# Kernel optimization log

Measured on AMD Instinct MI355X. Metric: run time of the kernel, lower is better.

## Reference

```python
import jax, jax.numpy as jnp
import numpy as np

N_NODES = 200000
N_EDGES = 600000
D_IN = 128
D_HID = 128
D_OUT = 100
NUM_GRAPHS = 2048
BN_EPS = 1e-5


def setup_inputs() -> dict:
    key = jax.random.key(0)
    ks = jax.random.split(key, 10)
    atom_features = jax.random.normal(ks[0], (N_NODES, D_IN), dtype=jnp.float32)
    edge_index = jax.random.randint(ks[1], (2, N_EDGES), 0, N_NODES, dtype=jnp.int32)
    batch = jnp.sort(jax.random.randint(ks[2], (N_NODES,), 0, NUM_GRAPHS, dtype=jnp.int32))
    s1 = 1.0 / np.sqrt(D_IN)
    s2 = 1.0 / np.sqrt(D_HID)
    return {
        "atom_features": atom_features,
        "edge_index": edge_index,
        "batch": batch,
        "num_graphs": NUM_GRAPHS,
        "W1": jax.random.uniform(ks[3], (D_IN, D_HID), jnp.float32, -s1, s1),
        "b1": jnp.zeros((D_HID,), jnp.float32),
        "gamma": jnp.ones((D_HID,), jnp.float32),
        "beta": jnp.zeros((D_HID,), jnp.float32),
        "W2": jax.random.uniform(ks[4], (D_HID, D_OUT), jnp.float32, -s2, s2),
        "b2": jnp.zeros((D_OUT,), jnp.float32),
    }


def gcn_conv(x, src, dst, W, b, num_nodes):
    # GCNConv: D^{-1/2} (A + I) D^{-1/2} X W + b  (self-loops already appended to src/dst)
    h = x @ W  # [N, F]
    deg = jax.ops.segment_sum(jnp.ones_like(dst, dtype=h.dtype), dst, num_segments=num_nodes)
    dinv = jnp.where(deg > 0, jax.lax.rsqrt(deg), 0.0)
    norm = dinv[src] * dinv[dst]  # [E+N]
    msg = h[src] * norm[:, None]
    out = jax.ops.segment_sum(msg, dst, num_segments=num_nodes)
    return out + b


def batch_norm(x, gamma, beta):
    mu = jnp.mean(x, axis=0)
    var = jnp.mean(jnp.square(x - mu), axis=0)
    return (x - mu) * jax.lax.rsqrt(var + BN_EPS) * gamma + beta


def reference(atom_features, edge_index, batch, num_graphs, W1, b1, gamma, beta, W2, b2):
    n = atom_features.shape[0]
    loops = jnp.arange(n, dtype=edge_index.dtype)
    src = jnp.concatenate([edge_index[0], loops])
    dst = jnp.concatenate([edge_index[1], loops])
    x = gcn_conv(atom_features, src, dst, W1, b1, n)
    x = batch_norm(x, gamma, beta)
    x = jax.nn.relu(x)  # dropout is a no-op in eval
    x = gcn_conv(x, src, dst, W2, b2, n)
    # global max pool by graph id
    return jax.ops.segment_max(x, batch, num_segments=num_graphs)
```

## Files before the change

kernel.cpp:

```cpp
#include <hip/hip_runtime.h>
#include <hip/hip_bf16.h>

#define D_HID 128
#define D_OUT 100
#define BN_EPS 1e-5f
#define XP 136
#define ROWB 272

typedef short bf16x8 __attribute__((ext_vector_type(8)));
typedef float f32x4 __attribute__((ext_vector_type(4)));

__device__ __forceinline__ unsigned fmap(float f) {
    unsigned u = __float_as_uint(f);
    return (u & 0x80000000u) ? ~u : (u | 0x80000000u);
}
__device__ __forceinline__ float funmap(unsigned u) {
    return __uint_as_float((u & 0x80000000u) ? (u ^ 0x80000000u) : ~u);
}
#define NEG_INF_MAPPED 0x007FFFFFu

__device__ __forceinline__ unsigned short f2bf(float f) {
    unsigned u = __float_as_uint(f);
    return (unsigned short)((u + 0x7fffu + ((u >> 16) & 1u)) >> 16);
}
__device__ __forceinline__ unsigned packbf2(float x, float y) {
    return (unsigned)f2bf(x) | ((unsigned)f2bf(y) << 16);
}
__device__ __forceinline__ float2 unpackbf2(unsigned v) {
    float2 r;
    r.x = __uint_as_float(v << 16);
    r.y = __uint_as_float(v & 0xffff0000u);
    return r;
}

__global__ __launch_bounds__(256) void init_k(int* deg, int* cursor, unsigned* pool,
                                              float* bnsum, float* bnsq, int N, int P) {
    int i = blockIdx.x * 256 + threadIdx.x;
    if (i < N) { deg[i] = 0; cursor[i] = 0; }
    if (i < P) pool[i] = NEG_INF_MAPPED;
    if (i < 128) { bnsum[i] = 0.f; bnsq[i] = 0.f; }
}

__global__ __launch_bounds__(256) void deg_k(const int* __restrict__ dst, int* deg, int E) {
    int e = blockIdx.x * 256 + threadIdx.x;
    if (e < E) atomicAdd(&deg[dst[e]], 1);
}

#define SCAN_EPB 1024
__global__ __launch_bounds__(256) void scan1_k(const int* __restrict__ deg, int* __restrict__ off,
                                               int* __restrict__ btot, int N) {
    __shared__ int ts[256];
    int base = blockIdx.x * SCAN_EPB + threadIdx.x * 4;
    int v[4];
    int s = 0;
#pragma unroll
    for (int j = 0; j < 4; ++j) { int idx = base + j; v[j] = (idx < N) ? deg[idx] : 0; s += v[j]; }
    ts[threadIdx.x] = s;
    __syncthreads();
    for (int d = 1; d < 256; d <<= 1) {
        int t = (threadIdx.x >= d) ? ts[threadIdx.x - d] : 0;
        __syncthreads();
        ts[threadIdx.x] += t;
        __syncthreads();
    }
    int excl = ts[threadIdx.x] - s;
#pragma unroll
    for (int j = 0; j < 4; ++j) { int idx = base + j; if (idx < N) off[idx] = excl; excl += v[j]; }
    if (threadIdx.x == 255) btot[blockIdx.x] = ts[255];
}

__global__ __launch_bounds__(256) void scan2_k(int* btot, int nb, int* off, int N, int E) {
    __shared__ int ts[256];
    int v = (threadIdx.x < nb) ? btot[threadIdx.x] : 0;
    ts[threadIdx.x] = v;
    __syncthreads();
    for (int d = 1; d < 256; d <<= 1) {
        int t = (threadIdx.x >= d) ? ts[threadIdx.x - d] : 0;
        __syncthreads();
        ts[threadIdx.x] += t;
        __syncthreads();
    }
    if (threadIdx.x < nb) btot[threadIdx.x] = ts[threadIdx.x] - v;
    if (threadIdx.x == 0) off[N] = E;
}

__global__ __launch_bounds__(256) void scan3_dinv_k(int* off, const int* __restrict__ btot,
                                                    const int* __restrict__ deg,
                                                    float* __restrict__ dinv, int N) {
    int i = blockIdx.x * 256 + threadIdx.x;
    if (i < N) {
        off[i] += btot[i / SCAN_EPB];
        dinv[i] = rsqrtf((float)(1 + deg[i]));
    }
}

__global__ __launch_bounds__(256) void fill_k(const int* __restrict__ src, const int* __restrict__ dst,
                                              const int* __restrict__ off, int* cursor,
                                              int* __restrict__ csr, int E) {
    int e = blockIdx.x * 256 + threadIdx.x;
    if (e < E) {
        int d = dst[e];
        int p = atomicAdd(&cursor[d], 1);
        csr[off[d] + p] = src[e];
    }
}

__global__ __launch_bounds__(256) void prepW_k(const float* __restrict__ W1,
                                               const float* __restrict__ W2,
                                               unsigned short* __restrict__ W1t,
                                               unsigned short* __restrict__ W2t) {
    int t = blockIdx.x * 256 + threadIdx.x;
    if (t < 16384) { int n = t >> 7, k = t & 127; W1t[t] = f2bf(W1[k * 128 + n]); }
    if (t < 14336) { int c = t >> 7, k = t & 127; W2t[t] = (c < D_OUT) ? f2bf(W2[k * D_OUT + c]) : (unsigned short)0; }
}

__global__ __launch_bounds__(256) void gemm1_k(const float* __restrict__ X,
                                               const unsigned short* __restrict__ W1t,
                                               const float* __restrict__ dinv,
                                               unsigned* __restrict__ H, int N) {
    __shared__ char smem[64 * ROWB + 128 * ROWB];
    char* Xs = smem;
    char* Wt = smem + 64 * ROWB;
    int tid = threadIdx.x;
    int row0 = blockIdx.x * 64;
    {
        const uint4* Wg = (const uint4*)W1t;
#pragma unroll
        for (int i = 0; i < 8; ++i) {
            int idx = i * 256 + tid;
            uint4 u = Wg[idx];
            *(uint4*)(Wt + (idx >> 4) * ROWB + (idx & 15) * 16) = u;
        }
    }
    {
        const float4* Xg = (const float4*)X;
#pragma unroll
        for (int i = 0; i < 8; ++i) {
            int idx = i * 256 + tid;
            int r = idx >> 5, c4 = idx & 31;
            int grow = row0 + r; if (grow >= N) grow = N - 1;
            float4 v = Xg[(long long)grow * 32 + c4];
            uint2 o; o.x = packbf2(v.x, v.y); o.y = packbf2(v.z, v.w);
            *(uint2*)(Xs + r * ROWB + c4 * 8) = o;
        }
    }
    __syncthreads();
    int w = tid >> 6, l = tid & 63;
    int arow = w * 16 + (l & 15);
    int koff = (l >> 4) * 16;
    f32x4 acc[8];
#pragma unroll
    for (int ct = 0; ct < 8; ++ct)
#pragma unroll
        for (int r = 0; r < 4; ++r) acc[ct][r] = 0.f;
#pragma unroll
    for (int ks = 0; ks < 4; ++ks) {
        int kb = ks * 64 + koff;
        bf16x8 a = *(const bf16x8*)(Xs + arow * ROWB + kb);
#pragma unroll
        for (int ct = 0; ct < 8; ++ct) {
            bf16x8 b = *(const bf16x8*)(Wt + (ct * 16 + (l & 15)) * ROWB + kb);
            acc[ct] = __builtin_amdgcn_mfma_f32_16x16x32_bf16(a, b, acc[ct], 0, 0, 0);
        }
    }
    __syncthreads();
    {
        int crow0 = w * 16 + (l >> 4) * 4;
        int ccol = l & 15;
#pragma unroll
        for (int ct = 0; ct < 8; ++ct)
#pragma unroll
            for (int r = 0; r < 4; ++r)
                *(unsigned short*)(Xs + (crow0 + r) * ROWB + (ct * 16 + ccol) * 2) = f2bf(acc[ct][r]);
    }
    __syncthreads();
#pragma unroll
    for (int i = 0; i < 16; ++i) {
        int idx = i * 256 + tid;
        int r = idx >> 6, cu = idx & 63;
        int grow = row0 + r;
        if (grow < N) {
            float2 f = unpackbf2(*(unsigned*)(Xs + r * ROWB + cu * 4));
            float d = dinv[grow];
            H[(long long)grow * 64 + cu] = packbf2(f.x * d, f.y * d);
        }
    }
}

#define A1_FLUSH_ADV()                                                  \
    do {                                                                \
        float ox = dncur * acc.x, oy = dncur * acc.y;                   \
        X1[(long long)n * 64 + lane] = packbf2(ox, oy);                 \
        bs.x += ox; bs.y += oy;                                         \
        bq.x += ox * ox; bq.y += oy * oy;                               \
        ++n;                                                            \
        nend = off[n + 1];                                              \
        dncur = dinv[n];                                                \
        acc = unpackbf2(hnext);                                         \
        int np_ = (n + 1 < N) ? (n + 1) : (N - 1);                      \
        hnext = H[(long long)np_ * 64 + lane];                          \
    } while (0)

__global__ __launch_bounds__(256) void agg1_k(const unsigned* __restrict__ H,
                                              const int* __restrict__ off,
                                              const int* __restrict__ csr,
                                              const float* __restrict__ dinv,
                                              unsigned* __restrict__ X1,
                                              float* bnsum, float* bnsq,
                                              int N, int chunk) {
    int grp = blockIdx.x * 4 + (threadIdx.x >> 6);
    int lane = threadIdx.x & 63;
    int n0 = grp * chunk;
    int n1 = n0 + chunk; if (n1 > N) n1 = N;
    float2 bs; bs.x = 0.f; bs.y = 0.f;
    float2 bq; bq.x = 0.f; bq.y = 0.f;
    if (n0 < n1) {
        int n = n0;
        int i = off[n0];
        int eend = off[n1];
        int nend = off[n0 + 1];
        float dncur = dinv[n0];
        float2 acc = unpackbf2(H[(long long)n0 * 64 + lane]);
        int np0 = (n0 + 1 < N) ? (n0 + 1) : (N - 1);
        unsigned hnext = H[(long long)np0 * 64 + lane];
        while (i + 4 <= eend) {
            int s0 = csr[i], s1 = csr[i + 1], s2 = csr[i + 2], s3 = csr[i + 3];
            unsigned g0 = H[(long long)s0 * 64 + lane];
            unsigned g1 = H[(long long)s1 * 64 + lane];
            unsigned g2 = H[(long long)s2 * 64 + lane];
            unsigned g3 = H[(long long)s3 * 64 + lane];
            while (i >= nend) A1_FLUSH_ADV();
            { float2 f = unpackbf2(g0); acc.x += f.x; acc.y += f.y; }
            while (i + 1 >= nend) A1_FLUSH_ADV();
            { float2 f = unpackbf2(g1); acc.x += f.x; acc.y += f.y; }
            while (i + 2 >= nend) A1_FLUSH_ADV();
            { float2 f = unpackbf2(g2); acc.x += f.x; acc.y += f.y; }
            while (i + 3 >= nend) A1_FLUSH_ADV();
            { float2 f = unpackbf2(g3); acc.x += f.x; acc.y += f.y; }
            i += 4;
        }
        while (i < eend) {
            int s0 = csr[i];
            unsigned g0 = H[(long long)s0 * 64 + lane];
            while (i >= nend) A1_FLUSH_ADV();
            { float2 f = unpackbf2(g0); acc.x += f.x; acc.y += f.y; }
            ++i;
        }
        for (;;) {
            float ox = dncur * acc.x, oy = dncur * acc.y;
            X1[(long long)n * 64 + lane] = packbf2(ox, oy);
            bs.x += ox; bs.y += oy;
            bq.x += ox * ox; bq.y += oy * oy;
            ++n;
            if (n >= n1) break;
            dncur = dinv[n];
            acc = unpackbf2(hnext);
            int np_ = (n + 1 < N) ? (n + 1) : (N - 1);
            hnext = H[(long long)np_ * 64 + lane];
        }
    }
    __shared__ float2 ls[256], lq[256];
    ls[threadIdx.x] = bs; lq[threadIdx.x] = bq;
    __syncthreads();
    if (threadIdx.x < 64) {
        float2 s = ls[threadIdx.x], q = lq[threadIdx.x];
#pragma unroll
        for (int j = 64; j < 256; j += 64) {
            float2 a = ls[threadIdx.x + j], b = lq[threadIdx.x + j];
            s.x += a.x; s.y += a.y; q.x += b.x; q.y += b.y;
        }
        atomicAdd(&bnsum[threadIdx.x * 2 + 0], s.x);
        atomicAdd(&bnsum[threadIdx.x * 2 + 1], s.y);
        atomicAdd(&bnsq[threadIdx.x * 2 + 0], q.x);
        atomicAdd(&bnsq[threadIdx.x * 2 + 1], q.y);
    }
}

__global__ __launch_bounds__(128) void bnfinal_k(const float* bnsum, const float* bnsq,
                                                 const float* __restrict__ gamma,
                                                 const float* __restrict__ beta,
                                                 float* scale, float* shift, int N) {
    int c = threadIdx.x;
    float mu = bnsum[c] / (float)N;
    float var = bnsq[c] / (float)N - mu * mu;
    var = var > 0.f ? var : 0.f;
    float sc = gamma[c] * rsqrtf(var + BN_EPS);
    scale[c] = sc;
    shift[c] = beta[c] - mu * sc;
}

__global__ __launch_bounds__(256) void gemm2_k(const unsigned* __restrict__ X1,
                                               const unsigned short* __restrict__ W2t,
                                               const float* __restrict__ scale,
                                               const float* __restrict__ shift,
                                               const float* __restrict__ dinv,
                                               unsigned* __restrict__ H2, int N) {
    __shared__ char smem[64 * ROWB + 112 * ROWB];
    __shared__ float scs[128], shs[128];
    char* Xs = smem;
    char* Wt = smem + 64 * ROWB;
    int tid = threadIdx.x;
    int row0 = blockIdx.x * 64;
    if (tid < 128) { scs[tid] = scale[tid]; shs[tid] = shift[tid]; }
    {
        const uint4* Wg = (const uint4*)W2t;
#pragma unroll
        for (int i = 0; i < 7; ++i) {
            int idx = i * 256 + tid;
            uint4 u = Wg[idx];
            *(uint4*)(Wt + (idx >> 4) * ROWB + (idx & 15) * 16) = u;
        }
    }
    __syncthreads();
    {
        const uint4* Xg = (const uint4*)X1;
#pragma unroll
        for (int i = 0; i < 4; ++i) {
            int idx = i * 256 + tid;
            int r = idx >> 4, kc = idx & 15;
            int grow = row0 + r; if (grow >= N) grow = N - 1;
            uint4 u = Xg[(long long)grow * 16 + kc];
            uint4 o;
#pragma unroll
            for (int jj = 0; jj < 4; ++jj) {
                float2 f = unpackbf2((&u.x)[jj]);
                int k = kc * 8 + jj * 2;
                float v0 = f.x * scs[k] + shs[k];
                float v1 = f.y * scs[k + 1] + shs[k + 1];
                (&o.x)[jj] = packbf2(v0 > 0.f ? v0 : 0.f, v1 > 0.f ? v1 : 0.f);
            }
            *(uint4*)(Xs + r * ROWB + kc * 16) = o;
        }
    }
    __syncthreads();
    int w = tid >> 6, l = tid & 63;
    int arow = w * 16 + (l & 15);
    int koff = (l >> 4) * 16;
    f32x4 acc[7];
#pragma unroll
    for (int ct = 0; ct < 7; ++ct)
#pragma unroll
        for (int r = 0; r < 4; ++r) acc[ct][r] = 0.f;
#pragma unroll
    for (int ks = 0; ks < 4; ++ks) {
        int kb = ks * 64 + koff;
        bf16x8 a = *(const bf16x8*)(Xs + arow * ROWB + kb);
#pragma unroll
        for (int ct = 0; ct < 7; ++ct) {
            bf16x8 b = *(const bf16x8*)(Wt + (ct * 16 + (l & 15)) * ROWB + kb);
            acc[ct] = __builtin_amdgcn_mfma_f32_16x16x32_bf16(a, b, acc[ct], 0, 0, 0);
        }
    }
    __syncthreads();
    {
        int crow0 = w * 16 + (l >> 4) * 4;
        int ccol = l & 15;
#pragma unroll
        for (int ct = 0; ct < 7; ++ct)
#pragma unroll
            for (int r = 0; r < 4; ++r)
                *(unsigned short*)(Xs + (crow0 + r) * ROWB + (ct * 16 + ccol) * 2) = f2bf(acc[ct][r]);
    }
    __syncthreads();
#pragma unroll
    for (int i = 0; i < 13; ++i) {
        int idx = i * 256 + tid;
        if (idx < 3200) {
            int r = idx / 50, cu = idx - r * 50;
            int grow = row0 + r;
            if (grow < N) {
                float2 f = unpackbf2(*(unsigned*)(Xs + r * ROWB + cu * 4));
                float d = dinv[grow];
                H2[(long long)grow * 50 + cu] = packbf2(f.x * d, f.y * d);
            }
        }
    }
}

#define NINF (-__builtin_inff())
#define A2_FLUSH_ADV()                                                  \
    do {                                                                \
        float vx_ = dncur * acc.x + bf.x, vy_ = dncur * acc.y + bf.y;   \
        int gb_ = batch[n];                                             \
        if (gb_ != gcur) {                                              \
            long long pb_ = (long long)gcur * D_OUT + lane * 2;         \
            atomicMax(&pool[pb_], fmap(mx));                            \
            atomicMax(&pool[pb_ + 1], fmap(my));                        \
            gcur = gb_; mx = NINF; my = NINF;                           \
        }                                                               \
        mx = mx > vx_ ? mx : vx_; my = my > vy_ ? my : vy_;             \
        ++n;                                                            \
        nend = off[n + 1];                                              \
        dncur = dinv[n];                                                \
        acc = unpackbf2(hnext);                                         \
        int np_ = (n + 1 < N) ? (n + 1) : (N - 1);                      \
        hnext = H2[(long long)np_ * 50 + lane];                         \
    } while (0)

__global__ __launch_bounds__(256) void agg2pool_k(const unsigned* __restrict__ H2,
                                                  const int* __restrict__ off,
                                                  const int* __restrict__ csr,
                                                  const float* __restrict__ dinv,
                                                  const int* __restrict__ batch,
                                                  const float* __restrict__ b2,
                                                  unsigned* __restrict__ pool,
                                                  int N, int chunk) {
    int grp = blockIdx.x * 4 + (threadIdx.x >> 6);
    int lane = threadIdx.x & 63;
    if (lane >= 50) return;
    int n0 = grp * chunk;
    int n1 = n0 + chunk; if (n1 > N) n1 = N;
    if (n0 >= n1) return;
    float2 bf = ((const float2*)b2)[lane];
    float mx = NINF, my = NINF;
    int gcur = batch[n0];
    int n = n0;
    int i = off[n0];
    int eend = off[n1];
    int nend = off[n0 + 1];
    float dncur = dinv[n0];
    float2 acc = unpackbf2(H2[(long long)n0 * 50 + lane]);
    int np0 = (n0 + 1 < N) ? (n0 + 1) : (N - 1);
    unsigned hnext = H2[(long long)np0 * 50 + lane];
    while (i + 4 <= eend) {
        int s0 = csr[i], s1 = csr[i + 1], s2 = csr[i + 2], s3 = csr[i + 3];
        unsigned g0 = H2[(long long)s0 * 50 + lane];
        unsigned g1 = H2[(long long)s1 * 50 + lane];
        unsigned g2 = H2[(long long)s2 * 50 + lane];
        unsigned g3 = H2[(long long)s3 * 50 + lane];
        while (i >= nend) A2_FLUSH_ADV();
        { float2 f = unpackbf2(g0); acc.x += f.x; acc.y += f.y; }
        while (i + 1 >= nend) A2_FLUSH_ADV();
        { float2 f = unpackbf2(g1); acc.x += f.x; acc.y += f.y; }
        while (i + 2 >= nend) A2_FLUSH_ADV();
        { float2 f = unpackbf2(g2); acc.x += f.x; acc.y += f.y; }
        while (i + 3 >= nend) A2_FLUSH_ADV();
        { float2 f = unpackbf2(g3); acc.x += f.x; acc.y += f.y; }
        i += 4;
    }
    while (i < eend) {
        int s0 = csr[i];
        unsigned g0 = H2[(long long)s0 * 50 + lane];
        while (i >= nend) A2_FLUSH_ADV();
        { float2 f = unpackbf2(g0); acc.x += f.x; acc.y += f.y; }
        ++i;
    }
    for (;;) {
        float vx_ = dncur * acc.x + bf.x, vy_ = dncur * acc.y + bf.y;
        int gb_ = batch[n];
        if (gb_ != gcur) {
            long long pb_ = (long long)gcur * D_OUT + lane * 2;
            atomicMax(&pool[pb_], fmap(mx));
            atomicMax(&pool[pb_ + 1], fmap(my));
            gcur = gb_; mx = NINF; my = NINF;
        }
        mx = mx > vx_ ? mx : vx_; my = my > vy_ ? my : vy_;
        ++n;
        if (n >= n1) break;
        dncur = dinv[n];
        acc = unpackbf2(hnext);
        int np_ = (n + 1 < N) ? (n + 1) : (N - 1);
        hnext = H2[(long long)np_ * 50 + lane];
    }
    long long pb = (long long)gcur * D_OUT + lane * 2;
    atomicMax(&pool[pb], fmap(mx));
    atomicMax(&pool[pb + 1], fmap(my));
}

__global__ __launch_bounds__(256) void pool_final_k(const unsigned* __restrict__ pool,
                                                    float* __restrict__ out, int P) {
    int i = blockIdx.x * 256 + threadIdx.x;
    if (i < P) out[i] = funmap(pool[i]);
}

extern "C" void kernel_launch(void* const* d_in, const int* in_sizes, int n_in,
                              void* d_out, int out_size, void* d_ws, size_t ws_size,
                              hipStream_t stream) {
    const float* X     = (const float*)d_in[0];
    const int*   eidx  = (const int*)d_in[1];
    const int*   batch = (const int*)d_in[2];
    const float* W1    = (const float*)d_in[4];
    const float* gamma = (const float*)d_in[6];
    const float* beta  = (const float*)d_in[7];
    const float* W2    = (const float*)d_in[8];
    const float* b2    = (const float*)d_in[9];

    const int N = in_sizes[0] / D_HID;
    const int E = in_sizes[1] / 2;
    const int P = out_size;
    const int* src = eidx;
    const int* dst = eidx + E;

    char* p = (char*)d_ws;
    auto alloc = [&](size_t bytes) { char* q = p; p += (bytes + 255) & ~(size_t)255; return q; };
    int*      deg    = (int*)alloc((size_t)N * 4);
    int*      cursor = (int*)alloc((size_t)N * 4);
    int*      off    = (int*)alloc((size_t)(N + 1) * 4);
    int*      btot   = (int*)alloc(256 * 4);
    int*      csr    = (int*)alloc((size_t)E * 4);
    float*    dinv   = (float*)alloc((size_t)N * 4);
    float*    bnsum  = (float*)alloc(128 * 4);
    float*    bnsq   = (float*)alloc(128 * 4);
    float*    scale  = (float*)alloc(128 * 4);
    float*    shift  = (float*)alloc(128 * 4);
    unsigned short* W1t = (unsigned short*)alloc(16384 * 2);
    unsigned short* W2t = (unsigned short*)alloc(14336 * 2);
    unsigned* pool   = (unsigned*)alloc((size_t)P * 4);
    unsigned* A      = (unsigned*)alloc((size_t)N * 128 * 2);
    unsigned* B      = (unsigned*)alloc((size_t)N * 128 * 2);

    const int nb1 = (N + SCAN_EPB - 1) / SCAN_EPB;
    const int initN = (N > P ? N : P);

    init_k<<<(initN + 255) / 256, 256, 0, stream>>>(deg, cursor, pool, bnsum, bnsq, N, P);
    deg_k<<<(E + 255) / 256, 256, 0, stream>>>(dst, deg, E);
    scan1_k<<<nb1, 256, 0, stream>>>(deg, off, btot, N);
    scan2_k<<<1, 256, 0, stream>>>(btot, nb1, off, N, E);
    scan3_dinv_k<<<(N + 255) / 256, 256, 0, stream>>>(off, btot, deg, dinv, N);
    fill_k<<<(E + 255) / 256, 256, 0, stream>>>(src, dst, off, cursor, csr, E);
    prepW_k<<<64, 256, 0, stream>>>(W1, W2, W1t, W2t);

    const int nblk_g = (N + 63) / 64;
    gemm1_k<<<nblk_g, 256, 0, stream>>>(X, W1t, dinv, A, N);

    const int nblk_agg = 2048;
    const int ngrp = nblk_agg * 4;
    const int chunk = (N + ngrp - 1) / ngrp;
    agg1_k<<<nblk_agg, 256, 0, stream>>>(A, off, csr, dinv, B, bnsum, bnsq, N, chunk);
    bnfinal_k<<<1, 128, 0, stream>>>(bnsum, bnsq, gamma, beta, scale, shift, N);

    gemm2_k<<<nblk_g, 256, 0, stream>>>(B, W2t, scale, shift, dinv, A, N);

    agg2pool_k<<<nblk_agg, 256, 0, stream>>>(A, off, csr, dinv, batch, b2, pool, N, chunk);
    pool_final_k<<<(P + 255) / 256, 256, 0, stream>>>(pool, (float*)d_out, P);
}
```

Measured before the change: 313.1 us.

## Pad CSR to even degree and gather two edges per wavefront with half-wave lanes

Each node's CSR neighbour list is padded to an even length, using a dummy node whose feature row is zero. Each wavefront then processes edge pairs: each half-wave gathers one source row with 8-byte loads, and the two halves are summed with a cross-lane shuffle before the node's output is written. The goal is to halve the number of serial gather iterations and widen the memory accesses in both aggregation kernels. The cost is extra padding work, a new pad kernel, idle lanes in the second layer's 25-of-32 layout, and shuffles on every node flush.

Measured after the change: 419.4 us. 34.0% more time.

```diff
diff --git a/kernel.cpp b/kernel.cpp
--- a/kernel.cpp
+++ b/kernel.cpp
@@ -32,13 +32,20 @@
     r.y = __uint_as_float(v & 0xffff0000u);
     return r;
 }
+__device__ __forceinline__ f32x4 unpack4(uint2 u) {
+    float2 a = unpackbf2(u.x), b = unpackbf2(u.y);
+    f32x4 r; r[0] = a.x; r[1] = a.y; r[2] = b.x; r[3] = b.y;
+    return r;
+}
 
 __global__ __launch_bounds__(256) void init_k(int* deg, int* cursor, unsigned* pool,
-                                              float* bnsum, float* bnsq, int N, int P) {
+                                              float* bnsum, float* bnsq,
+                                              unsigned* Hpad, int N, int P) {
     int i = blockIdx.x * 256 + threadIdx.x;
     if (i < N) { deg[i] = 0; cursor[i] = 0; }
     if (i < P) pool[i] = NEG_INF_MAPPED;
     if (i < 128) { bnsum[i] = 0.f; bnsq[i] = 0.f; }
+    if (i < 64) Hpad[i] = 0;
 }
 
 __global__ __launch_bounds__(256) void deg_k(const int* __restrict__ dst, int* deg, int E) {
@@ -54,7 +61,12 @@
     int v[4];
     int s = 0;
 #pragma unroll
-    for (int j = 0; j < 4; ++j) { int idx = base + j; v[j] = (idx < N) ? deg[idx] : 0; s += v[j]; }
+    for (int j = 0; j < 4; ++j) {
+        int idx = base + j;
+        int d = (idx < N) ? deg[idx] : 0;
+        v[j] = d + (d & 1);
+        s += v[j];
+    }
     ts[threadIdx.x] = s;
     __syncthreads();
     for (int d = 1; d < 256; d <<= 1) {
@@ -69,7 +81,7 @@
     if (threadIdx.x == 255) btot[blockIdx.x] = ts[255];
 }
 
-__global__ __launch_bounds__(256) void scan2_k(int* btot, int nb, int* off, int N, int E) {
+__global__ __launch_bounds__(256) void scan2_k(int* btot, int nb, int* off, int N) {
     __shared__ int ts[256];
     int v = (threadIdx.x < nb) ? btot[threadIdx.x] : 0;
     ts[threadIdx.x] = v;
@@ -81,7 +93,7 @@
         __syncthreads();
     }
     if (threadIdx.x < nb) btot[threadIdx.x] = ts[threadIdx.x] - v;
-    if (threadIdx.x == 0) off[N] = E;
+    if (threadIdx.x == 255) off[N] = ts[255];
 }
 
 __global__ __launch_bounds__(256) void scan3_dinv_k(int* off, const int* __restrict__ btot,
@@ -102,6 +114,15 @@
         int d = dst[e];
         int p = atomicAdd(&cursor[d], 1);
         csr[off[d] + p] = src[e];
+    }
+}
+
+__global__ __launch_bounds__(256) void pad_k(const int* __restrict__ deg, const int* __restrict__ off,
+                                             int* __restrict__ csr, int N) {
+    int i = blockIdx.x * 256 + threadIdx.x;
+    if (i < N) {
+        int d = deg[i];
+        if (d & 1) csr[off[i] + d] = N;
     }
 }
 
@@ -187,100 +208,127 @@
     }
 }
 
-#define A1_FLUSH_ADV()                                                  \
-    do {                                                                \
-        float ox = dncur * acc.x, oy = dncur * acc.y;                   \
-        X1[(long long)n * 64 + lane] = packbf2(ox, oy);                 \
-        bs.x += ox; bs.y += oy;                                         \
-        bq.x += ox * ox; bq.y += oy * oy;                               \
-        ++n;                                                            \
-        nend = off[n + 1];                                              \
-        dncur = dinv[n];                                                \
-        acc = unpackbf2(hnext);                                         \
-        int np_ = (n + 1 < N) ? (n + 1) : (N - 1);                      \
-        hnext = H[(long long)np_ * 64 + lane];                          \
+#define A1_FLUSH_ADV()                                                      \
+    do {                                                                    \
+        f32x4 tot;                                                          \
+        tot[0] = acc[0] + __shfl(acc[0], lane + 32);                        \
+        tot[1] = acc[1] + __shfl(acc[1], lane + 32);                        \
+        tot[2] = acc[2] + __shfl(acc[2], lane + 32);                        \
+        tot[3] = acc[3] + __shfl(acc[3], lane + 32);                        \
+        if (lo) {                                                           \
+            f32x4 ox;                                                       \
+            ox[0] = dncur * tot[0]; ox[1] = dncur * tot[1];                 \
+            ox[2] = dncur * tot[2]; ox[3] = dncur * tot[3];                 \
+            uint2 o; o.x = packbf2(ox[0], ox[1]); o.y = packbf2(ox[2], ox[3]); \
+            X1v[(long long)n * 32 + hl] = o;                                \
+            bs += ox; bq += ox * ox;                                        \
+        }                                                                   \
+        ++n;                                                                \
+        pn = off[n + 1] >> 1;                                               \
+        dncur = dinv[n];                                                    \
+        if (lo) acc = unpack4(hnext); else { acc[0]=0.f;acc[1]=0.f;acc[2]=0.f;acc[3]=0.f; } \
+        int np_ = (n + 1 < N) ? (n + 1) : (N - 1);                          \
+        hnext = Hv[(long long)np_ * 32 + hl];                               \
     } while (0)
 
-__global__ __launch_bounds__(256) void agg1_k(const unsigned* __restrict__ H,
+__global__ __launch_bounds__(256) void agg1_k(const uint2* __restrict__ Hv,
                                               const int* __restrict__ off,
-                                              const int* __restrict__ csr,
+                                              const int2* __restrict__ csr2,
                                               const float* __restrict__ dinv,
-                                              unsigned* __restrict__ X1,
+                                              uint2* __restrict__ X1v,
                                               float* bnsum, float* bnsq,
                                               int N, int chunk) {
     int grp = blockIdx.x * 4 + (threadIdx.x >> 6);
     int lane = threadIdx.x & 63;
+    int hl = lane & 31;
+    bool lo = lane < 32;
     int n0 = grp * chunk;
     int n1 = n0 + chunk; if (n1 > N) n1 = N;
-    float2 bs; bs.x = 0.f; bs.y = 0.f;
-    float2 bq; bq.x = 0.f; bq.y = 0.f;
+    f32x4 bs; bs[0]=0.f;bs[1]=0.f;bs[2]=0.f;bs[3]=0.f;
+    f32x4 bq = bs;
     if (n0 < n1) {
         int n = n0;
-        int i = off[n0];
-        int eend = off[n1];
-        int nend = off[n0 + 1];
+        int pi = off[n0] >> 1;
+        int pe = off[n1] >> 1;
+        int pn = off[n0 + 1] >> 1;
         float dncur = dinv[n0];
-        float2 acc = unpackbf2(H[(long long)n0 * 64 + lane]);
+        f32x4 acc;
+        {
+            uint2 hs = Hv[(long long)n0 * 32 + hl];
+            if (lo) acc = unpack4(hs); else { acc[0]=0.f;acc[1]=0.f;acc[2]=0.f;acc[3]=0.f; }
+        }
         int np0 = (n0 + 1 < N) ? (n0 + 1) : (N - 1);
-        unsigned hnext = H[(long long)np0 * 64 + lane];
-        while (i + 4 <= eend) {
-            int s0 = csr[i], s1 = csr[i + 1], s2 = csr[i + 2], s3 = csr[i + 3];
-            unsigned g0 = H[(long long)s0 * 64 + lane];
-            unsigned g1 = H[(long long)s1 * 64 + lane];
-            unsigned g2 = H[(long long)s2 * 64 + lane];
-            unsigned g3 = H[(long long)s3 * 64 + lane];
-            while (i >= nend) A1_FLUSH_ADV();
-            { float2 f = unpackbf2(g0); acc.x += f.x; acc.y += f.y; }
-            while (i + 1 >= nend) A1_FLUSH_ADV();
-            { float2 f = unpackbf2(g1); acc.x += f.x; acc.y += f.y; }
-            while (i + 2 >= nend) A1_FLUSH_ADV();
-            { float2 f = unpackbf2(g2); acc.x += f.x; acc.y += f.y; }
-            while (i + 3 >= nend) A1_FLUSH_ADV();
-            { float2 f = unpackbf2(g3); acc.x += f.x; acc.y += f.y; }
-            i += 4;
-        }
-        while (i < eend) {
-            int s0 = csr[i];
-            unsigned g0 = H[(long long)s0 * 64 + lane];
-            while (i >= nend) A1_FLUSH_ADV();
-            { float2 f = unpackbf2(g0); acc.x += f.x; acc.y += f.y; }
-            ++i;
+        uint2 hnext = Hv[(long long)np0 * 32 + hl];
+        while (pi + 4 <= pe) {
+            int2 e0 = csr2[pi], e1 = csr2[pi + 1], e2 = csr2[pi + 2], e3 = csr2[pi + 3];
+            int s0 = lo ? e0.x : e0.y, s1 = lo ? e1.x : e1.y;
+            int s2 = lo ? e2.x : e2.y, s3 = lo ? e3.x : e3.y;
+            uint2 g0 = Hv[(long long)s0 * 32 + hl];
+            uint2 g1 = Hv[(long long)s1 * 32 + hl];
+            uint2 g2 = Hv[(long long)s2 * 32 + hl];
+            uint2 g3 = Hv[(long long)s3 * 32 + hl];
+            while (pi >= pn) A1_FLUSH_ADV();
+            acc += unpack4(g0);
+            while (pi + 1 >= pn) A1_FLUSH_ADV();
+            acc += unpack4(g1);
+            while (pi + 2 >= pn) A1_FLUSH_ADV();
+            acc += unpack4(g2);
+            while (pi + 3 >= pn) A1_FLUSH_ADV();
+            acc += unpack4(g3);
+            pi += 4;
+        }
+        while (pi < pe) {
+            int2 e0 = csr2[pi];
+            int s0 = lo ? e0.x : e0.y;
+            uint2 g0 = Hv[(long long)s0 * 32 + hl];
+            while (pi >= pn) A1_FLUSH_ADV();
+            acc += unpack4(g0);
+            ++pi;
         }
         for (;;) {
-            float ox = dncur * acc.x, oy = dncur * acc.y;
-            X1[(long long)n * 64 + lane] = packbf2(ox, oy);
-            bs.x += ox; bs.y += oy;
-            bq.x += ox * ox; bq.y += oy * oy;
+            f32x4 tot;
+            tot[0] = acc[0] + __shfl(acc[0], lane + 32);
+            tot[1] = acc[1] + __shfl(acc[1], lane + 32);
+            tot[2] = acc[2] + __shfl(acc[2], lane + 32);
+            tot[3] = acc[3] + __shfl(acc[3], lane + 32);
+            if (lo) {
+                f32x4 ox;
+                ox[0] = dncur * tot[0]; ox[1] = dncur * tot[1];
+                ox[2] = dncur * tot[2]; ox[3] = dncur * tot[3];
+                uint2 o; o.x = packbf2(ox[0], ox[1]); o.y = packbf2(ox[2], ox[3]);
+                X1v[(long long)n * 32 + hl] = o;
+                bs += ox; bq += ox * ox;
+            }
             ++n;
             if (n >= n1) break;
             dncur = dinv[n];
-            acc = unpackbf2(hnext);
+            if (lo) acc = unpack4(hnext); else { acc[0]=0.f;acc[1]=0.f;acc[2]=0.f;acc[3]=0.f; }
             int np_ = (n + 1 < N) ? (n + 1) : (N - 1);
-            hnext = H[(long long)np_ * 64 + lane];
-        }
-    }
-    __shared__ float2 ls[256], lq[256];
+            hnext = Hv[(long long)np_ * 32 + hl];
+        }
+    }
+    __shared__ f32x4 ls[256], lq[256];
     ls[threadIdx.x] = bs; lq[threadIdx.x] = bq;
     __syncthreads();
-    if (threadIdx.x < 64) {
-        float2 s = ls[threadIdx.x], q = lq[threadIdx.x];
-#pragma unroll
-        for (int j = 64; j < 256; j += 64) {
-            float2 a = ls[threadIdx.x + j], b = lq[threadIdx.x + j];
-            s.x += a.x; s.y += a.y; q.x += b.x; q.y += b.y;
-        }
-        atomicAdd(&bnsum[threadIdx.x * 2 + 0], s.x);
-        atomicAdd(&bnsum[threadIdx.x * 2 + 1], s.y);
-        atomicAdd(&bnsq[threadIdx.x * 2 + 0], q.x);
-        atomicAdd(&bnsq[threadIdx.x * 2 + 1], q.y);
+    if (threadIdx.x < 32) {
+        f32x4 s = ls[threadIdx.x], q = lq[threadIdx.x];
+#pragma unroll
+        for (int j = 32; j < 256; j += 32) { s += ls[threadIdx.x + j]; q += lq[threadIdx.x + j]; }
+        int f = threadIdx.x * 4;
+        atomicAdd(&bnsum[f + 0], s[0]); atomicAdd(&bnsum[f + 1], s[1]);
+        atomicAdd(&bnsum[f + 2], s[2]); atomicAdd(&bnsum[f + 3], s[3]);
+        atomicAdd(&bnsq[f + 0], q[0]);  atomicAdd(&bnsq[f + 1], q[1]);
+        atomicAdd(&bnsq[f + 2], q[2]);  atomicAdd(&bnsq[f + 3], q[3]);
     }
 }
 
 __global__ __launch_bounds__(128) void bnfinal_k(const float* bnsum, const float* bnsq,
                                                  const float* __restrict__ gamma,
                                                  const float* __restrict__ beta,
-                                                 float* scale, float* shift, int N) {
+                                                 float* scale, float* shift,
+                                                 unsigned* H2pad, int N) {
     int c = threadIdx.x;
+    if (c < 50) H2pad[c] = 0;
     float mu = bnsum[c] / (float)N;
     float var = bnsq[c] / (float)N - mu * mu;
     var = var > 0.f ? var : 0.f;
@@ -378,28 +426,42 @@
 }
 
 #define NINF (-__builtin_inff())
-#define A2_FLUSH_ADV()                                                  \
-    do {                                                                \
-        float vx_ = dncur * acc.x + bf.x, vy_ = dncur * acc.y + bf.y;   \
-        int gb_ = batch[n];                                             \
-        if (gb_ != gcur) {                                              \
-            long long pb_ = (long long)gcur * D_OUT + lane * 2;         \
-            atomicMax(&pool[pb_], fmap(mx));                            \
-            atomicMax(&pool[pb_ + 1], fmap(my));                        \
-            gcur = gb_; mx = NINF; my = NINF;                           \
-        }                                                               \
-        mx = mx > vx_ ? mx : vx_; my = my > vy_ ? my : vy_;             \
-        ++n;                                                            \
-        nend = off[n + 1];                                              \
-        dncur = dinv[n];                                                \
-        acc = unpackbf2(hnext);                                         \
-        int np_ = (n + 1 < N) ? (n + 1) : (N - 1);                      \
-        hnext = H2[(long long)np_ * 50 + lane];                         \
+#define A2_FLUSH_ADV()                                                      \
+    do {                                                                    \
+        f32x4 tot;                                                          \
+        tot[0] = acc[0] + __shfl(acc[0], lane + 32);                        \
+        tot[1] = acc[1] + __shfl(acc[1], lane + 32);                        \
+        tot[2] = acc[2] + __shfl(acc[2], lane + 32);                        \
+        tot[3] = acc[3] + __shfl(acc[3], lane + 32);                        \
+        int gb_ = batch[n];                                                 \
+        if (gb_ != gcur) {                                                  \
+            if (valid) {                                                    \
+                long long pb_ = (long long)gcur * D_OUT + hl * 4;           \
+                atomicMax(&pool[pb_ + 0], fmap(mx[0]));                     \
+                atomicMax(&pool[pb_ + 1], fmap(mx[1]));                     \
+                atomicMax(&pool[pb_ + 2], fmap(mx[2]));                     \
+                atomicMax(&pool[pb_ + 3], fmap(mx[3]));                     \
+            }                                                               \
+            gcur = gb_;                                                     \
+            mx[0]=NINF; mx[1]=NINF; mx[2]=NINF; mx[3]=NINF;                 \
+        }                                                                   \
+        if (valid) {                                                        \
+            float v0 = dncur * tot[0] + bf.x, v1 = dncur * tot[1] + bf.y;   \
+            float v2 = dncur * tot[2] + bf.z, v3 = dncur * tot[3] + bf.w;   \
+            mx[0] = mx[0] > v0 ? mx[0] : v0; mx[1] = mx[1] > v1 ? mx[1] : v1; \
+            mx[2] = mx[2] > v2 ? mx[2] : v2; mx[3] = mx[3] > v3 ? mx[3] : v3; \
+        }                                                                   \
+        ++n;                                                                \
+        pn = off[n + 1] >> 1;                                               \
+        dncur = dinv[n];                                                    \
+        if (lo) acc = unpack4(hnext); else { acc[0]=0.f;acc[1]=0.f;acc[2]=0.f;acc[3]=0.f; } \
+        int np_ = (n + 1 < N) ? (n + 1) : (N - 1);                          \
+        hnext = H2v[(long long)np_ * 25 + idx25];                           \
     } while (0)
 
-__global__ __launch_bounds__(256) void agg2pool_k(const unsigned* __restrict__ H2,
+__global__ __launch_bounds__(256) void agg2pool_k(const uint2* __restrict__ H2v,
                                                   const int* __restrict__ off,
-                                                  const int* __restrict__ csr,
+                                                  const int2* __restrict__ csr2,
                                                   const float* __restrict__ dinv,
                                                   const int* __restrict__ batch,
                                                   const float* __restrict__ b2,
@@ -407,64 +469,93 @@
                                                   int N, int chunk) {
     int grp = blockIdx.x * 4 + (threadIdx.x >> 6);
     int lane = threadIdx.x & 63;
-    if (lane >= 50) return;
+    int hl = lane & 31;
+    bool lo = lane < 32;
+    bool valid = lo && (hl < 25);
+    int idx25 = hl < 25 ? hl : 24;
     int n0 = grp * chunk;
     int n1 = n0 + chunk; if (n1 > N) n1 = N;
     if (n0 >= n1) return;
-    float2 bf = ((const float2*)b2)[lane];
-    float mx = NINF, my = NINF;
+    float4 bf;
+    if (hl < 25) bf = ((const float4*)b2)[hl]; else { bf.x=0;bf.y=0;bf.z=0;bf.w=0; }
+    f32x4 mx; mx[0]=NINF; mx[1]=NINF; mx[2]=NINF; mx[3]=NINF;
     int gcur = batch[n0];
     int n = n0;
-    int i = off[n0];
-    int eend = off[n1];
-    int nend = off[n0 + 1];
+    int pi = off[n0] >> 1;
+    int pe = off[n1] >> 1;
+    int pn = off[n0 + 1] >> 1;
     float dncur = dinv[n0];
-    float2 acc = unpackbf2(H2[(long long)n0 * 50 + lane]);
+    f32x4 acc;
+    {
+        uint2 hs = H2v[(long long)n0 * 25 + idx25];
+        if (lo) acc = unpack4(hs); else { acc[0]=0.f;acc[1]=0.f;acc[2]=0.f;acc[3]=0.f; }
+    }
     int np0 = (n0 + 1 < N) ? (n0 + 1) : (N - 1);
-    unsigned hnext = H2[(long long)np0 * 50 + lane];
-    while (i + 4 <= eend) {
-        int s0 = csr[i], s1 = csr[i + 1], s2 = csr[i + 2], s3 = csr[i + 3];
-        unsigned g0 = H2[(long long)s0 * 50 + lane];
-        unsigned g1 = H2[(long long)s1 * 50 + lane];
-        unsigned g2 = H2[(long long)s2 * 50 + lane];
-        unsigned g3 = H2[(long long)s3 * 50 + lane];
-        while (i >= nend) A2_FLUSH_ADV();
-        { float2 f = unpackbf2(g0); acc.x += f.x; acc.y += f.y; }
-        while (i + 1 >= nend) A2_FLUSH_ADV();
-        { float2 f = unpackbf2(g1); acc.x += f.x; acc.y += f.y; }
-        while (i + 2 >= nend) A2_FLUSH_ADV();
-        { float2 f = unpackbf2(g2); acc.x += f.x; acc.y += f.y; }
-        while (i + 3 >= nend) A2_FLUSH_ADV();
-        { float2 f = unpackbf2(g3); acc.x += f.x; acc.y += f.y; }
-        i += 4;
-    }
-    while (i < eend) {
-        int s0 = csr[i];
-        unsigned g0 = H2[(long long)s0 * 50 + lane];
-        while (i >= nend) A2_FLUSH_ADV();
-        { float2 f = unpackbf2(g0); acc.x += f.x; acc.y += f.y; }
-        ++i;
+    uint2 hnext = H2v[(long long)np0 * 25 + idx25];
+    while (pi + 4 <= pe) {
+        int2 e0 = csr2[pi], e1 = csr2[pi + 1], e2 = csr2[pi + 2], e3 = csr2[pi + 3];
+        int s0 = lo ? e0.x : e0.y, s1 = lo ? e1.x : e1.y;
+        int s2 = lo ? e2.x : e2.y, s3 = lo ? e3.x : e3.y;
+        uint2 g0 = H2v[(long long)s0 * 25 + idx25];
+        uint2 g1 = H2v[(long long)s1 * 25 + idx25];
+        uint2 g2 = H2v[(long long)s2 * 25 + idx25];
+        uint2 g3 = H2v[(long long)s3 * 25 + idx25];
+        while (pi >= pn) A2_FLUSH_ADV();
+        acc += unpack4(g0);
+        while (pi + 1 >= pn) A2_FLUSH_ADV();
+        acc += unpack4(g1);
+        while (pi + 2 >= pn) A2_FLUSH_ADV();
+        acc += unpack4(g2);
+        while (pi + 3 >= pn) A2_FLUSH_ADV();
+        acc += unpack4(g3);
+        pi += 4;
+    }
+    while (pi < pe) {
+        int2 e0 = csr2[pi];
+        int s0 = lo ? e0.x : e0.y;
+        uint2 g0 = H2v[(long long)s0 * 25 + idx25];
+        while (pi >= pn) A2_FLUSH_ADV();
+        acc += unpack4(g0);
+        ++pi;
     }
     for (;;) {
-        float vx_ = dncur * acc.x + bf.x, vy_ = dncur * acc.y + bf.y;
+        f32x4 tot;
+        tot[0] = acc[0] + __shfl(acc[0], lane + 32);
+        tot[1] = acc[1] + __shfl(acc[1], lane + 32);
+        tot[2] = acc[2] + __shfl(acc[2], lane + 32);
+        tot[3] = acc[3] + __shfl(acc[3], lane + 32);
         int gb_ = batch[n];
         if (gb_ != gcur) {
-            long long pb_ = (long long)gcur * D_OUT + lane * 2;
-            atomicMax(&pool[pb_], fmap(mx));
-            atomicMax(&pool[pb_ + 1], fmap(my));
-            gcur = gb_; mx = NINF; my = NINF;
-        }
-        mx = mx > vx_ ? mx : vx_; my = my > vy_ ? my : vy_;
+            if (valid) {
+                long long pb_ = (long long)gcur * D_OUT + hl * 4;
+                atomicMax(&pool[pb_ + 0], fmap(mx[0]));
+                atomicMax(&pool[pb_ + 1], fmap(mx[1]));
+                atomicMax(&pool[pb_ + 2], fmap(mx[2]));
+                atomicMax(&pool[pb_ + 3], fmap(mx[3]));
+            }
+            gcur = gb_;
+            mx[0]=NINF; mx[1]=NINF; mx[2]=NINF; mx[3]=NINF;
+        }
+        if (valid) {
+            float v0 = dncur * tot[0] + bf.x, v1 = dncur * tot[1] + bf.y;
+            float v2 = dncur * tot[2] + bf.z, v3 = dncur * tot[3] + bf.w;
+            mx[0] = mx[0] > v0 ? mx[0] : v0; mx[1] = mx[1] > v1 ? mx[1] : v1;
+            mx[2] = mx[2] > v2 ? mx[2] : v2; mx[3] = mx[3] > v3 ? mx[3] : v3;
+        }
         ++n;
         if (n >= n1) break;
         dncur = dinv[n];
-        acc = unpackbf2(hnext);
+        if (lo) acc = unpack4(hnext); else { acc[0]=0.f;acc[1]=0.f;acc[2]=0.f;acc[3]=0.f; }
         int np_ = (n + 1 < N) ? (n + 1) : (N - 1);
-        hnext = H2[(long long)np_ * 50 + lane];
-    }
-    long long pb = (long long)gcur * D_OUT + lane * 2;
-    atomicMax(&pool[pb], fmap(mx));
-    atomicMax(&pool[pb + 1], fmap(my));
+        hnext = H2v[(long long)np_ * 25 + idx25];
+    }
+    if (valid) {
+        long long pb = (long long)gcur * D_OUT + hl * 4;
+        atomicMax(&pool[pb + 0], fmap(mx[0]));
+        atomicMax(&pool[pb + 1], fmap(mx[1]));
+        atomicMax(&pool[pb + 2], fmap(mx[2]));
+        atomicMax(&pool[pb + 3], fmap(mx[3]));
+    }
 }
 
 __global__ __launch_bounds__(256) void pool_final_k(const unsigned* __restrict__ pool,
@@ -497,7 +588,7 @@
     int*      cursor = (int*)alloc((size_t)N * 4);
     int*      off    = (int*)alloc((size_t)(N + 1) * 4);
     int*      btot   = (int*)alloc(256 * 4);
-    int*      csr    = (int*)alloc((size_t)E * 4);
+    int*      csr    = (int*)alloc((size_t)(E + N + 2) * 4);
     float*    dinv   = (float*)alloc((size_t)N * 4);
     float*    bnsum  = (float*)alloc(128 * 4);
     float*    bnsq   = (float*)alloc(128 * 4);
@@ -506,18 +597,20 @@
     unsigned short* W1t = (unsigned short*)alloc(16384 * 2);
     unsigned short* W2t = (unsigned short*)alloc(14336 * 2);
     unsigned* pool   = (unsigned*)alloc((size_t)P * 4);
-    unsigned* A      = (unsigned*)alloc((size_t)N * 128 * 2);
+    unsigned* A      = (unsigned*)alloc((size_t)(N + 1) * 128 * 2);
     unsigned* B      = (unsigned*)alloc((size_t)N * 128 * 2);
 
     const int nb1 = (N + SCAN_EPB - 1) / SCAN_EPB;
     const int initN = (N > P ? N : P);
 
-    init_k<<<(initN + 255) / 256, 256, 0, stream>>>(deg, cursor, pool, bnsum, bnsq, N, P);
+    init_k<<<(initN + 255) / 256, 256, 0, stream>>>(deg, cursor, pool, bnsum, bnsq,
+                                                    A + (size_t)N * 64, N, P);
     deg_k<<<(E + 255) / 256, 256, 0, stream>>>(dst, deg, E);
     scan1_k<<<nb1, 256, 0, stream>>>(deg, off, btot, N);
-    scan2_k<<<1, 256, 0, stream>>>(btot, nb1, off, N, E);
+    scan2_k<<<1, 256, 0, stream>>>(btot, nb1, off, N);
     scan3_dinv_k<<<(N + 255) / 256, 256, 0, stream>>>(off, btot, deg, dinv, N);
     fill_k<<<(E + 255) / 256, 256, 0, stream>>>(src, dst, off, cursor, csr, E);
+    pad_k<<<(N + 255) / 256, 256, 0, stream>>>(deg, off, csr, N);
     prepW_k<<<64, 256, 0, stream>>>(W1, W2, W1t, W2t);
 
     const int nblk_g = (N + 63) / 64;
@@ -526,11 +619,14 @@
     const int nblk_agg = 2048;
     const int ngrp = nblk_agg * 4;
     const int chunk = (N + ngrp - 1) / ngrp;
-    agg1_k<<<nblk_agg, 256, 0, stream>>>(A, off, csr, dinv, B, bnsum, bnsq, N, chunk);
-    bnfinal_k<<<1, 128, 0, stream>>>(bnsum, bnsq, gamma, beta, scale, shift, N);
+    agg1_k<<<nblk_agg, 256, 0, stream>>>((const uint2*)A, off, (const int2*)csr, dinv,
+                                         (uint2*)B, bnsum, bnsq, N, chunk);
+    bnfinal_k<<<1, 128, 0, stream>>>(bnsum, bnsq, gamma, beta, scale, shift,
+                                     A + (size_t)N * 50, N);
 
     gemm2_k<<<nblk_g, 256, 0, stream>>>(B, W2t, scale, shift, dinv, A, N);
 
-    agg2pool_k<<<nblk_agg, 256, 0, stream>>>(A, off, csr, dinv, batch, b2, pool, N, chunk);
+    agg2pool_k<<<nblk_agg, 256, 0, stream>>>((const uint2*)A, off, (const int2*)csr, dinv,
+                                             batch, b2, pool, N, chunk);
     pool_final_k<<<(P + 255) / 256, 256, 0, stream>>>(pool, (float*)d_out, P);
 }
```
